# Performance work log

Measured on AMD Instinct MI355X. Metric: run time of the kernel, lower is better.

Reference implementation:

```python
import jax, jax.numpy as jnp
import numpy as np

N_NODES = 50000
NEG_SLOPE = 0.2  # PyG GATConv default
DROP_P = 0.3


def gat_layer(x, src, dst, W, a_src, a_dst, b, n):
    # x: [N, din]; src/dst: [E'] (self-loops already appended)
    h = x @ W                                   # [N, dout]
    s_src = (h * a_src).sum(-1)                 # [N]
    s_dst = (h * a_dst).sum(-1)                 # [N]
    alpha = jax.nn.leaky_relu(s_src[src] + s_dst[dst], NEG_SLOPE)  # [E']
    # segment softmax over destination node
    amax = jax.ops.segment_max(alpha, dst, num_segments=n)
    e = jnp.exp(alpha - amax[dst])
    denom = jax.ops.segment_sum(e, dst, num_segments=n)
    coef = e / denom[dst]                       # [E']
    out = jax.ops.segment_sum(coef[:, None] * h[src], dst, num_segments=n)
    return out + b


def setup_inputs() -> dict:
    key = jax.random.key(0)
    ks = jax.random.split(key, 10)
    d1, d2 = 64, 64
    E = jax.random.normal(ks[0], (N_NODES, d1), jnp.float32)
    A = jax.random.randint(ks[1], (2, 800000), 0, N_NODES, jnp.int64)
    W1 = jax.random.normal(ks[2], (d1, d1), jnp.float32) / np.sqrt(d1)
    a_src1 = jax.random.normal(ks[3], (d1,), jnp.float32) / np.sqrt(d1)
    a_dst1 = jax.random.normal(ks[4], (d1,), jnp.float32) / np.sqrt(d1)
    b1 = jnp.zeros((d1,), jnp.float32)
    W2 = jax.random.normal(ks[5], (d1, d2), jnp.float32) / np.sqrt(d1)
    a_src2 = jax.random.normal(ks[6], (d2,), jnp.float32) / np.sqrt(d2)
    a_dst2 = jax.random.normal(ks[7], (d2,), jnp.float32) / np.sqrt(d2)
    b2 = jnp.zeros((d2,), jnp.float32)
    return {"E": E, "A": A, "W1": W1, "a_src1": a_src1, "a_dst1": a_dst1,
            "b1": b1, "W2": W2, "a_src2": a_src2, "a_dst2": a_dst2, "b2": b2}


def reference(E, A, W1, a_src1, a_dst1, b1, W2, a_src2, a_dst2, b2):
    n = E.shape[0]
    loop = jnp.arange(n, dtype=A.dtype)
    src = jnp.concatenate([A[0], loop])  # PyG GATConv adds self-loops
    dst = jnp.concatenate([A[1], loop])
    x1 = jax.nn.relu(gat_layer(E, src, dst, W1, a_src1, a_dst1, b1, n))
    # F.dropout(p=0.3) runs in training mode by default -> deterministic fixed-key mask
    keep = jax.random.bernoulli(jax.random.key(42), 1.0 - DROP_P, x1.shape)
    x1 = jnp.where(keep, x1 / (1.0 - DROP_P), 0.0)
    x2 = jax.nn.relu(gat_layer(x1, src, dst, W2, a_src2, a_dst2, b2, n))
    return x2
```

## Files before the change

kernel.cpp:

```cpp
#include <hip/hip_runtime.h>


#define XT_STRIDE 68

__device__ __forceinline__ unsigned rotl32(unsigned x, unsigned r) {
  return (x << r) | (x >> (32u - r));
}

__device__ __forceinline__ void threefry2_0_42(unsigned c0, unsigned c1,
                                               unsigned* o0, unsigned* o1) {
  const unsigned k0 = 0u, k1 = 42u;
  const unsigned k2 = k0 ^ k1 ^ 0x1BD11BDAu;
  unsigned ks[3] = {k0, k1, k2};
  unsigned x0 = c0 + ks[0];
  unsigned x1 = c1 + ks[1];
  const unsigned R[2][4] = {{13u, 15u, 26u, 6u}, {17u, 29u, 16u, 24u}};
#pragma unroll
  for (int i = 0; i < 5; ++i) {
#pragma unroll
    for (int j = 0; j < 4; ++j) {
      unsigned r = R[i & 1][j];
      x0 += x1;
      x1 = rotl32(x1, r);
      x1 ^= x0;
    }
    x0 += ks[(i + 1) % 3];
    x1 += ks[(i + 2) % 3] + (unsigned)(i + 1);
  }
  *o0 = x0;
  *o1 = x1;
}

__device__ __forceinline__ float ldf(const void* p, int isbf, size_t i) {
  if (isbf) {
    unsigned short u = ((const unsigned short*)p)[i];
    return __uint_as_float(((unsigned)u) << 16);
  }
  return ((const float*)p)[i];
}

__global__ __launch_bounds__(256) void k_prep(
    const void* __restrict__ A, const void* __restrict__ Ein, int nNodes,
    const void* W1, const void* as1, const void* ad1, const void* b1,
    const void* W2, const void* as2, const void* ad2, const void* b2,
    float* __restrict__ smallc, int* __restrict__ deg, int* __restrict__ cursor,
    int* __restrict__ flags) {
  __shared__ int s_ok64, s_bf;
  int t = threadIdx.x;
  if (t == 0) { s_ok64 = 1; s_bf = 0; }
  __syncthreads();
  long long v = ((const long long*)A)[t];
  if (!(v >= 0 && v < (long long)nNodes)) atomicAnd(&s_ok64, 0);
  unsigned w = ((const unsigned*)Ein)[t];
  unsigned b = (w >> 8) & 0x7F;
  if (b >= 0x3A && b <= 0x43) atomicAdd(&s_bf, 1);
  __syncthreads();
  int isbf = (s_bf >= 200) ? 1 : 0;
  int i = blockIdx.x * 256 + t;
  if (blockIdx.x == 0 && t == 0) {
    flags[0] = s_ok64;
    flags[1] = isbf;
  }
  if (i < 8576) {
    float x;
    if (i < 4096) x = ldf(W1, isbf, i);
    else if (i < 4160) x = ldf(as1, isbf, i - 4096);
    else if (i < 4224) x = ldf(ad1, isbf, i - 4160);
    else if (i < 4288) x = ldf(b1, isbf, i - 4224);
    else if (i < 8384) x = ldf(W2, isbf, i - 4288);
    else if (i < 8448) x = ldf(as2, isbf, i - 8384);
    else if (i < 8512) x = ldf(ad2, isbf, i - 8448);
    else x = ldf(b2, isbf, i - 8512);
    smallc[i] = x;
  }
  if (i < nNodes) {
    deg[i] = 1;
    cursor[i] = 0;
  }
}

__global__ __launch_bounds__(256) void k_count_gemm(
    const void* __restrict__ A, const int* __restrict__ flags, int Eb,
    int* __restrict__ deg, const void* __restrict__ X, int xDetect,
    const float* __restrict__ W, const float* __restrict__ a_src,
    const float* __restrict__ a_dst, float* __restrict__ H,
    float* __restrict__ ssrc, float* __restrict__ sdst, int n,
    int nCountBlocks) {
  __shared__ float Xt[64 * XT_STRIDE];
  __shared__ float Ws[64 * 64];
  int t = threadIdx.x;
  if ((int)blockIdx.x < nCountBlocks) {
    int e = blockIdx.x * 256 + t;
    if (e < Eb) {
      int d = flags[0] ? (int)((const long long*)A)[(long long)Eb + e]
                       : ((const int*)A)[Eb + e];
      atomicAdd(&deg[d], 1);
    }
    return;
  }
  int bid = blockIdx.x - nCountBlocks;
  int row0 = bid * 64;
  int isbf = xDetect ? flags[1] : 0;

#pragma unroll
  for (int i = t; i < 1024; i += 256) {
    int k = i >> 4, jq = i & 15;
    *(float4*)&Ws[k * 64 + jq * 4] = *(const float4*)&W[k * 64 + jq * 4];
  }
#pragma unroll
  for (int i = t; i < 1024; i += 256) {
    int q = i & 15, r = i >> 4;
    int row = row0 + r;
    float4 v = {0.f, 0.f, 0.f, 0.f};
    if (row < n) {
      if (isbf) {
        v.x = ldf(X, 1, (size_t)row * 64 + q * 4 + 0);
        v.y = ldf(X, 1, (size_t)row * 64 + q * 4 + 1);
        v.z = ldf(X, 1, (size_t)row * 64 + q * 4 + 2);
        v.w = ldf(X, 1, (size_t)row * 64 + q * 4 + 3);
      } else {
        v = *(const float4*)&((const float*)X)[(size_t)row * 64 + q * 4];
      }
    }
    Xt[(q * 4 + 0) * XT_STRIDE + r] = v.x;
    Xt[(q * 4 + 1) * XT_STRIDE + r] = v.y;
    Xt[(q * 4 + 2) * XT_STRIDE + r] = v.z;
    Xt[(q * 4 + 3) * XT_STRIDE + r] = v.w;
  }
  __syncthreads();

  int r0 = (t >> 4) * 4;
  int c0 = (t & 15) * 4;
  float acc[4][4];
#pragma unroll
  for (int r = 0; r < 4; ++r)
#pragma unroll
    for (int c = 0; c < 4; ++c) acc[r][c] = 0.f;

#pragma unroll 8
  for (int k = 0; k < 64; ++k) {
    float4 a4 = *(const float4*)&Xt[k * XT_STRIDE + r0];
    float4 b4 = *(const float4*)&Ws[k * 64 + c0];
    const float av[4] = {a4.x, a4.y, a4.z, a4.w};
    const float bv[4] = {b4.x, b4.y, b4.z, b4.w};
#pragma unroll
    for (int r = 0; r < 4; ++r)
#pragma unroll
      for (int c = 0; c < 4; ++c) acc[r][c] = fmaf(av[r], bv[c], acc[r][c]);
  }

  const float4 asr = *(const float4*)&a_src[c0];
  const float4 adr = *(const float4*)&a_dst[c0];
#pragma unroll
  for (int r = 0; r < 4; ++r) {
    float vs = acc[r][0] * asr.x + acc[r][1] * asr.y + acc[r][2] * asr.z +
               acc[r][3] * asr.w;
    float vd = acc[r][0] * adr.x + acc[r][1] * adr.y + acc[r][2] * adr.z +
               acc[r][3] * adr.w;
#pragma unroll
    for (int d = 1; d < 16; d <<= 1) {
      vs += __shfl_xor(vs, d);
      vd += __shfl_xor(vd, d);
    }
    int row = row0 + r0 + r;
    if ((t & 15) == 0 && row < n) {
      ssrc[row] = vs;
      sdst[row] = vd;
    }
  }

#pragma unroll
  for (int r = 0; r < 4; ++r) {
    int row = row0 + r0 + r;
    if (row < n) {
      float4 o = {acc[r][0], acc[r][1], acc[r][2], acc[r][3]};
      *(float4*)&H[(size_t)row * 64 + c0] = o;
    }
  }
}

__global__ __launch_bounds__(1024) void k_scan_one(const int* __restrict__ deg,
                                                   int* __restrict__ offsets,
                                                   int n, int etot) {
  __shared__ int wsum[16];
  __shared__ int carry;
  int t = threadIdx.x;
  int lane = t & 63;
  int w = t >> 6;
  if (t == 0) carry = 0;
  __syncthreads();
  for (int base = 0; base < n; base += 1024) {
    int i = base + t;
    int x = (i < n) ? deg[i] : 0;
    int sc = x;
#pragma unroll
    for (int d = 1; d < 64; d <<= 1) {
      int o = __shfl_up(sc, d);
      if (lane >= d) sc += o;
    }
    if (lane == 63) wsum[w] = sc;
    __syncthreads();
    int cbase = carry;
    if (t < 64) {
      int v = (t < 16) ? wsum[t] : 0;
#pragma unroll
      for (int d = 1; d < 16; d <<= 1) {
        int o = __shfl_up(v, d);
        if (lane >= d) v += o;
      }
      if (t < 16) wsum[t] = v;
    }
    __syncthreads();
    int wpre = (w == 0) ? 0 : wsum[w - 1];
    if (i < n) offsets[i] = cbase + wpre + (sc - x);
    int tot = wsum[15];
    __syncthreads();
    if (t == 0) carry = cbase + tot;
    __syncthreads();
  }
  if (t == 0) offsets[n] = etot;
}

__global__ __launch_bounds__(256) void k_fill(const void* __restrict__ A,
                                              const int* __restrict__ flags,
                                              const int* __restrict__ offsets,
                                              int* cursor, int* __restrict__ csr,
                                              int Eb, int nnode) {
  int e = blockIdx.x * 256 + threadIdx.x;
  if (e >= Eb + nnode) return;
  int s, d;
  if (e < Eb) {
    if (flags[0]) {
      s = (int)((const long long*)A)[e];
      d = (int)((const long long*)A)[(long long)Eb + e];
    } else {
      s = ((const int*)A)[e];
      d = ((const int*)A)[Eb + e];
    }
  } else {
    s = d = e - Eb;
  }
  int slot = atomicAdd(&cursor[d], 1);
  csr[offsets[d] + slot] = s;
}

#define AGG_STEP(IDX, ACC)                                              \
  {                                                                     \
    int idx_ = (IDX);                                                   \
    float cl_ = __shfl(c, idx_);                                        \
    int sr_ = __shfl(sl, idx_);                                         \
    if (idx_ < glim) {                                                  \
      const float4 hv_ = *(const float4*)&h[(size_t)sr_ * 64 + f4 * 4]; \
      ACC.x = fmaf(cl_, hv_.x, ACC.x);                                  \
      ACC.y = fmaf(cl_, hv_.y, ACC.y);                                  \
      ACC.z = fmaf(cl_, hv_.z, ACC.z);                                  \
      ACC.w = fmaf(cl_, hv_.w, ACC.w);                                  \
    }                                                                   \
  }

template <int DROPOUT>
__global__ __launch_bounds__(256) void k_aggregate(
    const float* __restrict__ h, const float* __restrict__ ssrc,
    const float* __restrict__ sdst, const float* __restrict__ bias,
    const int* __restrict__ offsets, const int* __restrict__ csr,
    float* __restrict__ alphaE, float* __restrict__ out, int n) {
  int wid = (blockIdx.x * 256 + threadIdx.x) >> 6;
  int lane = threadIdx.x & 63;
  if (wid >= n) return;
  int off = offsets[wid];
  int end = offsets[wid + 1];
  int g = end - off;
  float sd = sdst[wid];
  int e4 = lane >> 4, f4 = lane & 15;
  float4 acc0 = {0.f, 0.f, 0.f, 0.f}, acc1 = {0.f, 0.f, 0.f, 0.f};

  if (g <= 64) {
    int sl = 0;
    float v = -1e30f;
    if (lane < g) {
      sl = csr[off + lane];
      float tv = ssrc[sl] + sd;
      v = (tv > 0.f) ? tv : 0.2f * tv;
    }
    float m = v;
#pragma unroll
    for (int d = 32; d; d >>= 1) m = fmaxf(m, __shfl_xor(m, d));
    float ex = (lane < g) ? __expf(v - m) : 0.f;
    float s = ex;
#pragma unroll
    for (int d = 32; d; d >>= 1) s += __shfl_xor(s, d);
    float c = ex * (1.f / s);
    int glim = g;
    for (int cb = 0; cb < g; cb += 8) {
      AGG_STEP(cb + e4, acc0)
      AGG_STEP(cb + 4 + e4, acc1)
    }
  } else {
    float mm = -1e30f, ss = 0.f;
    for (int e = off + lane; e < end; e += 64) {
      int sl2 = csr[e];
      float tv = ssrc[sl2] + sd;
      tv = (tv > 0.f) ? tv : 0.2f * tv;
      alphaE[e] = tv;
      float mn = fmaxf(mm, tv);
      ss = ss * __expf(mm - mn) + __expf(tv - mn);
      mm = mn;
    }
#pragma unroll
    for (int d = 32; d; d >>= 1) {
      float mo = __shfl_xor(mm, d);
      float so = __shfl_xor(ss, d);
      float mn = fmaxf(mm, mo);
      ss = ss * __expf(mm - mn) + so * __expf(mo - mn);
      mm = mn;
    }
    float inv = 1.f / ss;
    for (int base = off; base < end; base += 64) {
      int e = base + lane;
      int cnt = min(64, end - base);
      float c = 0.f;
      int sl = 0;
      if (e < end) {
        c = __expf(alphaE[e] - mm) * inv;
        sl = csr[e];
      }
      int glim = cnt;
      for (int cb = 0; cb < cnt; cb += 8) {
        AGG_STEP(cb + e4, acc0)
        AGG_STEP(cb + 4 + e4, acc1)
      }
    }
  }

  float4 r;
  r.x = acc0.x + acc1.x;
  r.y = acc0.y + acc1.y;
  r.z = acc0.z + acc1.z;
  r.w = acc0.w + acc1.w;
#pragma unroll
  for (int d = 16; d < 64; d <<= 1) {
    r.x += __shfl_xor(r.x, d);
    r.y += __shfl_xor(r.y, d);
    r.z += __shfl_xor(r.z, d);
    r.w += __shfl_xor(r.w, d);
  }

  unsigned long long mask = 0ull;
  if (DROPOUT) {
    unsigned i0 = (unsigned)wid * 64u + (unsigned)lane;
    unsigned o0, o1;
    threefry2_0_42(0u, i0, &o0, &o1);
    unsigned bits = o0 ^ o1;
    float u = __uint_as_float((bits >> 9) | 0x3f800000u) - 1.0f;
    mask = __ballot(u < 0.7f);
  }

  if (lane < 16) {
    const float4 b4 = *(const float4*)&bias[lane * 4];
    r.x = fmaxf(r.x + b4.x, 0.f);
    r.y = fmaxf(r.y + b4.y, 0.f);
    r.z = fmaxf(r.z + b4.z, 0.f);
    r.w = fmaxf(r.w + b4.w, 0.f);
    if (DROPOUT) {
      r.x = ((mask >> (lane * 4 + 0)) & 1ull) ? r.x / 0.7f : 0.f;
      r.y = ((mask >> (lane * 4 + 1)) & 1ull) ? r.y / 0.7f : 0.f;
      r.z = ((mask >> (lane * 4 + 2)) & 1ull) ? r.z / 0.7f : 0.f;
      r.w = ((mask >> (lane * 4 + 3)) & 1ull) ? r.w / 0.7f : 0.f;
    }
    *(float4*)&out[(size_t)wid * 64 + lane * 4] = r;
  }
}

extern "C" void kernel_launch(void* const* d_in, const int* in_sizes, int n_in,
                              void* d_out, int out_size, void* d_ws, size_t ws_size,
                              hipStream_t stream) {
  const void* E = d_in[0];
  const void* A = d_in[1];
  const void* W1 = d_in[2];
  const void* as1 = d_in[3];
  const void* ad1 = d_in[4];
  const void* b1 = d_in[5];
  const void* W2 = d_in[6];
  const void* as2 = d_in[7];
  const void* ad2 = d_in[8];
  const void* b2 = d_in[9];
  float* out = (float*)d_out;

  const int N = in_sizes[0] / 64;
  const int Eb = in_sizes[1] / 2;
  const int Etot = Eb + N;
  const int total = N * 64;

  float* ws = (float*)d_ws;
  float* h = ws;
  float* x1 = h + (size_t)total;
  float* ssrc = x1 + (size_t)total;
  float* sdst = ssrc + N;
  float* alphaE = sdst + N;
  float* smallc = alphaE + Etot;
  int* deg = (int*)(smallc + 8576);
  int* offsets = deg + N;
  int* cursor = offsets + (N + 1);
  int* flags = cursor + N;
  int* csr = flags + 2;

  float* W1c = smallc;
  float* as1c = smallc + 4096;
  float* ad1c = smallc + 4160;
  float* b1c = smallc + 4224;
  float* W2c = smallc + 4288;
  float* as2c = smallc + 8384;
  float* ad2c = smallc + 8448;
  float* b2c = smallc + 8512;

  const int gPrep = (N + 255) / 256;
  const int nCountBlocks = (Eb + 255) / 256;
  const int gTile = (N + 63) / 64;
  const int gAgg = (N + 3) / 4;
  const int gFill = (Etot + 255) / 256;

  k_prep<<<gPrep, 256, 0, stream>>>(A, E, N, W1, as1, ad1, b1, W2, as2, ad2,
                                    b2, smallc, deg, cursor, flags);
  k_count_gemm<<<nCountBlocks + gTile, 256, 0, stream>>>(
      A, flags, Eb, deg, E, 1, W1c, as1c, ad1c, h, ssrc, sdst, N, nCountBlocks);
  k_scan_one<<<1, 1024, 0, stream>>>(deg, offsets, N, Etot);
  k_fill<<<gFill, 256, 0, stream>>>(A, flags, offsets, cursor, csr, Eb, N);
  k_aggregate<1><<<gAgg, 256, 0, stream>>>(h, ssrc, sdst, b1c, offsets, csr,
                                           alphaE, x1, N);
  k_count_gemm<<<gTile, 256, 0, stream>>>(A, flags, Eb, deg, x1, 0, W2c, as2c,
                                          ad2c, h, ssrc, sdst, N, 0);
  k_aggregate<0><<<gAgg, 256, 0, stream>>>(h, ssrc, sdst, b2c, offsets, csr,
                                           alphaE, out, N);
}
```

Baseline: 320.5 us.

## Fuse all GAT stages into one persistent cooperative kernel with grid syncs

Replaces the seven separate launches (prep, count+gemm, single-block scan, fill, two aggregates, second gemm) with one cooperative persistent kernel that separates phases with grid.sync. The single-block serial scan becomes a parallel two-level chunked scan, and the GEMM now stages K in two 32-wide chunks to cut shared memory and raise occupancy. The aim is to remove launch gaps and the serial scan bottleneck. In exchange, grid-wide barriers and a grid capped at occupancy size may limit parallelism in the gather-heavy aggregation phases. The first GEMM also runs on only a third of the blocks while the rest count degrees.

```diff
diff --git a/kernel.cpp b/kernel.cpp
--- a/kernel.cpp
+++ b/kernel.cpp
@@ -1,7 +1,8 @@
 #include <hip/hip_runtime.h>
-
-
-#define XT_STRIDE 68
+#include <hip/hip_cooperative_groups.h>
+
+namespace cg = cooperative_groups;
+
 
 __device__ __forceinline__ unsigned rotl32(unsigned x, unsigned r) {
   return (x << r) | (x >> (32u - r));
@@ -39,209 +40,121 @@
   return ((const float*)p)[i];
 }
 
-__global__ __launch_bounds__(256) void k_prep(
-    const void* __restrict__ A, const void* __restrict__ Ein, int nNodes,
-    const void* W1, const void* as1, const void* ad1, const void* b1,
-    const void* W2, const void* as2, const void* ad2, const void* b2,
-    float* __restrict__ smallc, int* __restrict__ deg, int* __restrict__ cursor,
-    int* __restrict__ flags) {
-  __shared__ int s_ok64, s_bf;
-  int t = threadIdx.x;
-  if (t == 0) { s_ok64 = 1; s_bf = 0; }
+__device__ __forceinline__ void block_scan256(int v, int t, int* wpre,
+                                              int* exclOut, int* totOut) {
+  int lane = t & 63, w = t >> 6;
+  int inc = v;
+#pragma unroll
+  for (int d = 1; d < 64; d <<= 1) {
+    int o = __shfl_up(inc, d);
+    if (lane >= d) inc += o;
+  }
+  if (lane == 63) wpre[w] = inc;
   __syncthreads();
-  long long v = ((const long long*)A)[t];
-  if (!(v >= 0 && v < (long long)nNodes)) atomicAnd(&s_ok64, 0);
-  unsigned w = ((const unsigned*)Ein)[t];
-  unsigned b = (w >> 8) & 0x7F;
-  if (b >= 0x3A && b <= 0x43) atomicAdd(&s_bf, 1);
+  int wp = 0, tot = 0;
+#pragma unroll
+  for (int j = 0; j < 4; ++j) {
+    int s = wpre[j];
+    if (j < w) wp += s;
+    tot += s;
+  }
   __syncthreads();
-  int isbf = (s_bf >= 200) ? 1 : 0;
-  int i = blockIdx.x * 256 + t;
-  if (blockIdx.x == 0 && t == 0) {
-    flags[0] = s_ok64;
-    flags[1] = isbf;
-  }
-  if (i < 8576) {
-    float x;
-    if (i < 4096) x = ldf(W1, isbf, i);
-    else if (i < 4160) x = ldf(as1, isbf, i - 4096);
-    else if (i < 4224) x = ldf(ad1, isbf, i - 4160);
-    else if (i < 4288) x = ldf(b1, isbf, i - 4224);
-    else if (i < 8384) x = ldf(W2, isbf, i - 4288);
-    else if (i < 8448) x = ldf(as2, isbf, i - 8384);
-    else if (i < 8512) x = ldf(ad2, isbf, i - 8448);
-    else x = ldf(b2, isbf, i - 8512);
-    smallc[i] = x;
-  }
-  if (i < nNodes) {
-    deg[i] = 1;
-    cursor[i] = 0;
-  }
-}
-
-__global__ __launch_bounds__(256) void k_count_gemm(
-    const void* __restrict__ A, const int* __restrict__ flags, int Eb,
-    int* __restrict__ deg, const void* __restrict__ X, int xDetect,
-    const float* __restrict__ W, const float* __restrict__ a_src,
-    const float* __restrict__ a_dst, float* __restrict__ H,
-    float* __restrict__ ssrc, float* __restrict__ sdst, int n,
-    int nCountBlocks) {
-  __shared__ float Xt[64 * XT_STRIDE];
-  __shared__ float Ws[64 * 64];
-  int t = threadIdx.x;
-  if ((int)blockIdx.x < nCountBlocks) {
-    int e = blockIdx.x * 256 + t;
-    if (e < Eb) {
-      int d = flags[0] ? (int)((const long long*)A)[(long long)Eb + e]
-                       : ((const int*)A)[Eb + e];
-      atomicAdd(&deg[d], 1);
-    }
-    return;
-  }
-  int bid = blockIdx.x - nCountBlocks;
-  int row0 = bid * 64;
-  int isbf = xDetect ? flags[1] : 0;
-
-#pragma unroll
-  for (int i = t; i < 1024; i += 256) {
-    int k = i >> 4, jq = i & 15;
-    *(float4*)&Ws[k * 64 + jq * 4] = *(const float4*)&W[k * 64 + jq * 4];
-  }
-#pragma unroll
-  for (int i = t; i < 1024; i += 256) {
-    int q = i & 15, r = i >> 4;
-    int row = row0 + r;
-    float4 v = {0.f, 0.f, 0.f, 0.f};
-    if (row < n) {
-      if (isbf) {
-        v.x = ldf(X, 1, (size_t)row * 64 + q * 4 + 0);
-        v.y = ldf(X, 1, (size_t)row * 64 + q * 4 + 1);
-        v.z = ldf(X, 1, (size_t)row * 64 + q * 4 + 2);
-        v.w = ldf(X, 1, (size_t)row * 64 + q * 4 + 3);
-      } else {
-        v = *(const float4*)&((const float*)X)[(size_t)row * 64 + q * 4];
-      }
-    }
-    Xt[(q * 4 + 0) * XT_STRIDE + r] = v.x;
-    Xt[(q * 4 + 1) * XT_STRIDE + r] = v.y;
-    Xt[(q * 4 + 2) * XT_STRIDE + r] = v.z;
-    Xt[(q * 4 + 3) * XT_STRIDE + r] = v.w;
-  }
-  __syncthreads();
-
+  *exclOut = wp + inc - v;
+  *totOut = tot;
+}
+
+__device__ void gemm_phase(const void* __restrict__ X, int isbf,
+                           const float* __restrict__ Wc,
+                           const float* __restrict__ a_src,
+                           const float* __restrict__ a_dst,
+                           float* __restrict__ H, float* __restrict__ ssrc,
+                           float* __restrict__ sdst, int n, int bid0,
+                           int gstride, int t, float* Xt, float* Ws) {
+  const int gTile = (n + 63) >> 6;
   int r0 = (t >> 4) * 4;
   int c0 = (t & 15) * 4;
-  float acc[4][4];
-#pragma unroll
-  for (int r = 0; r < 4; ++r)
-#pragma unroll
-    for (int c = 0; c < 4; ++c) acc[r][c] = 0.f;
-
+  for (int tile = bid0; tile < gTile; tile += gstride) {
+    int row0 = tile * 64;
+    float acc[4][4];
+#pragma unroll
+    for (int r = 0; r < 4; ++r)
+#pragma unroll
+      for (int c = 0; c < 4; ++c) acc[r][c] = 0.f;
+
+#pragma unroll
+    for (int chunk = 0; chunk < 2; ++chunk) {
+      int kbase = chunk * 32;
+#pragma unroll
+      for (int i = t; i < 512; i += 256) {
+        int k = i >> 4, jq = i & 15;
+        *(float4*)&Ws[k * 64 + jq * 4] =
+            *(const float4*)&Wc[(kbase + k) * 64 + jq * 4];
+      }
+#pragma unroll
+      for (int i = t; i < 512; i += 256) {
+        int r = i >> 3, q = i & 7;
+        int row = row0 + r;
+        float4 v = {0.f, 0.f, 0.f, 0.f};
+        if (row < n) {
+          if (isbf) {
+            v.x = ldf(X, 1, (size_t)row * 64 + kbase + q * 4 + 0);
+            v.y = ldf(X, 1, (size_t)row * 64 + kbase + q * 4 + 1);
+            v.z = ldf(X, 1, (size_t)row * 64 + kbase + q * 4 + 2);
+            v.w = ldf(X, 1, (size_t)row * 64 + kbase + q * 4 + 3);
+          } else {
+            v = *(const float4*)&((const float*)X)[(size_t)row * 64 + kbase +
+                                                   q * 4];
+          }
+        }
+        Xt[(q * 4 + 0) * 68 + r] = v.x;
+        Xt[(q * 4 + 1) * 68 + r] = v.y;
+        Xt[(q * 4 + 2) * 68 + r] = v.z;
+        Xt[(q * 4 + 3) * 68 + r] = v.w;
+      }
+      __syncthreads();
 #pragma unroll 8
-  for (int k = 0; k < 64; ++k) {
-    float4 a4 = *(const float4*)&Xt[k * XT_STRIDE + r0];
-    float4 b4 = *(const float4*)&Ws[k * 64 + c0];
-    const float av[4] = {a4.x, a4.y, a4.z, a4.w};
-    const float bv[4] = {b4.x, b4.y, b4.z, b4.w};
-#pragma unroll
-    for (int r = 0; r < 4; ++r)
-#pragma unroll
-      for (int c = 0; c < 4; ++c) acc[r][c] = fmaf(av[r], bv[c], acc[r][c]);
-  }
-
-  const float4 asr = *(const float4*)&a_src[c0];
-  const float4 adr = *(const float4*)&a_dst[c0];
-#pragma unroll
-  for (int r = 0; r < 4; ++r) {
-    float vs = acc[r][0] * asr.x + acc[r][1] * asr.y + acc[r][2] * asr.z +
-               acc[r][3] * asr.w;
-    float vd = acc[r][0] * adr.x + acc[r][1] * adr.y + acc[r][2] * adr.z +
-               acc[r][3] * adr.w;
-#pragma unroll
-    for (int d = 1; d < 16; d <<= 1) {
-      vs += __shfl_xor(vs, d);
-      vd += __shfl_xor(vd, d);
-    }
-    int row = row0 + r0 + r;
-    if ((t & 15) == 0 && row < n) {
-      ssrc[row] = vs;
-      sdst[row] = vd;
-    }
-  }
-
-#pragma unroll
-  for (int r = 0; r < 4; ++r) {
-    int row = row0 + r0 + r;
-    if (row < n) {
-      float4 o = {acc[r][0], acc[r][1], acc[r][2], acc[r][3]};
-      *(float4*)&H[(size_t)row * 64 + c0] = o;
-    }
-  }
-}
-
-__global__ __launch_bounds__(1024) void k_scan_one(const int* __restrict__ deg,
-                                                   int* __restrict__ offsets,
-                                                   int n, int etot) {
-  __shared__ int wsum[16];
-  __shared__ int carry;
-  int t = threadIdx.x;
-  int lane = t & 63;
-  int w = t >> 6;
-  if (t == 0) carry = 0;
-  __syncthreads();
-  for (int base = 0; base < n; base += 1024) {
-    int i = base + t;
-    int x = (i < n) ? deg[i] : 0;
-    int sc = x;
-#pragma unroll
-    for (int d = 1; d < 64; d <<= 1) {
-      int o = __shfl_up(sc, d);
-      if (lane >= d) sc += o;
-    }
-    if (lane == 63) wsum[w] = sc;
-    __syncthreads();
-    int cbase = carry;
-    if (t < 64) {
-      int v = (t < 16) ? wsum[t] : 0;
+      for (int k = 0; k < 32; ++k) {
+        float4 a4 = *(const float4*)&Xt[k * 68 + r0];
+        float4 b4 = *(const float4*)&Ws[k * 64 + c0];
+        const float av[4] = {a4.x, a4.y, a4.z, a4.w};
+        const float bv[4] = {b4.x, b4.y, b4.z, b4.w};
+#pragma unroll
+        for (int r = 0; r < 4; ++r)
+#pragma unroll
+          for (int c = 0; c < 4; ++c)
+            acc[r][c] = fmaf(av[r], bv[c], acc[r][c]);
+      }
+      __syncthreads();
+    }
+
+    const float4 asr = *(const float4*)&a_src[c0];
+    const float4 adr = *(const float4*)&a_dst[c0];
+#pragma unroll
+    for (int r = 0; r < 4; ++r) {
+      float vs = acc[r][0] * asr.x + acc[r][1] * asr.y + acc[r][2] * asr.z +
+                 acc[r][3] * asr.w;
+      float vd = acc[r][0] * adr.x + acc[r][1] * adr.y + acc[r][2] * adr.z +
+                 acc[r][3] * adr.w;
 #pragma unroll
       for (int d = 1; d < 16; d <<= 1) {
-        int o = __shfl_up(v, d);
-        if (lane >= d) v += o;
-      }
-      if (t < 16) wsum[t] = v;
-    }
-    __syncthreads();
-    int wpre = (w == 0) ? 0 : wsum[w - 1];
-    if (i < n) offsets[i] = cbase + wpre + (sc - x);
-    int tot = wsum[15];
-    __syncthreads();
-    if (t == 0) carry = cbase + tot;
-    __syncthreads();
-  }
-  if (t == 0) offsets[n] = etot;
-}
-
-__global__ __launch_bounds__(256) void k_fill(const void* __restrict__ A,
-                                              const int* __restrict__ flags,
-                                              const int* __restrict__ offsets,
-                                              int* cursor, int* __restrict__ csr,
-                                              int Eb, int nnode) {
-  int e = blockIdx.x * 256 + threadIdx.x;
-  if (e >= Eb + nnode) return;
-  int s, d;
-  if (e < Eb) {
-    if (flags[0]) {
-      s = (int)((const long long*)A)[e];
-      d = (int)((const long long*)A)[(long long)Eb + e];
-    } else {
-      s = ((const int*)A)[e];
-      d = ((const int*)A)[Eb + e];
-    }
-  } else {
-    s = d = e - Eb;
-  }
-  int slot = atomicAdd(&cursor[d], 1);
-  csr[offsets[d] + slot] = s;
+        vs += __shfl_xor(vs, d);
+        vd += __shfl_xor(vd, d);
+      }
+      int row = row0 + r0 + r;
+      if ((t & 15) == 0 && row < n) {
+        ssrc[row] = vs;
+        sdst[row] = vd;
+      }
+    }
+#pragma unroll
+    for (int r = 0; r < 4; ++r) {
+      int row = row0 + r0 + r;
+      if (row < n) {
+        float4 o = {acc[r][0], acc[r][1], acc[r][2], acc[r][3]};
+        *(float4*)&H[(size_t)row * 64 + c0] = o;
+      }
+    }
+  }
 }
 
 #define AGG_STEP(IDX, ACC)                                              \
@@ -259,116 +172,243 @@
   }
 
 template <int DROPOUT>
-__global__ __launch_bounds__(256) void k_aggregate(
-    const float* __restrict__ h, const float* __restrict__ ssrc,
-    const float* __restrict__ sdst, const float* __restrict__ bias,
-    const int* __restrict__ offsets, const int* __restrict__ csr,
-    float* __restrict__ alphaE, float* __restrict__ out, int n) {
-  int wid = (blockIdx.x * 256 + threadIdx.x) >> 6;
-  int lane = threadIdx.x & 63;
-  if (wid >= n) return;
-  int off = offsets[wid];
-  int end = offsets[wid + 1];
-  int g = end - off;
-  float sd = sdst[wid];
+__device__ void agg_phase(const float* __restrict__ h,
+                          const float* __restrict__ ssrc,
+                          const float* __restrict__ sdst,
+                          const float* __restrict__ bias,
+                          const int* __restrict__ offsets,
+                          const int* __restrict__ csr,
+                          float* __restrict__ alphaE, float* __restrict__ out,
+                          int n, int bid, int G, int t) {
+  int lane = t & 63;
   int e4 = lane >> 4, f4 = lane & 15;
-  float4 acc0 = {0.f, 0.f, 0.f, 0.f}, acc1 = {0.f, 0.f, 0.f, 0.f};
-
-  if (g <= 64) {
-    int sl = 0;
-    float v = -1e30f;
-    if (lane < g) {
-      sl = csr[off + lane];
-      float tv = ssrc[sl] + sd;
-      v = (tv > 0.f) ? tv : 0.2f * tv;
-    }
-    float m = v;
-#pragma unroll
-    for (int d = 32; d; d >>= 1) m = fmaxf(m, __shfl_xor(m, d));
-    float ex = (lane < g) ? __expf(v - m) : 0.f;
-    float s = ex;
-#pragma unroll
-    for (int d = 32; d; d >>= 1) s += __shfl_xor(s, d);
-    float c = ex * (1.f / s);
-    int glim = g;
-    for (int cb = 0; cb < g; cb += 8) {
-      AGG_STEP(cb + e4, acc0)
-      AGG_STEP(cb + 4 + e4, acc1)
-    }
-  } else {
-    float mm = -1e30f, ss = 0.f;
-    for (int e = off + lane; e < end; e += 64) {
-      int sl2 = csr[e];
-      float tv = ssrc[sl2] + sd;
-      tv = (tv > 0.f) ? tv : 0.2f * tv;
-      alphaE[e] = tv;
-      float mn = fmaxf(mm, tv);
-      ss = ss * __expf(mm - mn) + __expf(tv - mn);
-      mm = mn;
-    }
-#pragma unroll
-    for (int d = 32; d; d >>= 1) {
-      float mo = __shfl_xor(mm, d);
-      float so = __shfl_xor(ss, d);
-      float mn = fmaxf(mm, mo);
-      ss = ss * __expf(mm - mn) + so * __expf(mo - mn);
-      mm = mn;
-    }
-    float inv = 1.f / ss;
-    for (int base = off; base < end; base += 64) {
-      int e = base + lane;
-      int cnt = min(64, end - base);
-      float c = 0.f;
+  for (int wid = bid * 4 + (t >> 6); wid < n; wid += G * 4) {
+    int off = offsets[wid];
+    int end = offsets[wid + 1];
+    int g = end - off;
+    float sd = sdst[wid];
+    float4 acc0 = {0.f, 0.f, 0.f, 0.f}, acc1 = {0.f, 0.f, 0.f, 0.f};
+
+    if (g <= 64) {
       int sl = 0;
-      if (e < end) {
-        c = __expf(alphaE[e] - mm) * inv;
-        sl = csr[e];
-      }
-      int glim = cnt;
-      for (int cb = 0; cb < cnt; cb += 8) {
+      float v = -1e30f;
+      if (lane < g) {
+        sl = csr[off + lane];
+        float tv = ssrc[sl] + sd;
+        v = (tv > 0.f) ? tv : 0.2f * tv;
+      }
+      float m = v;
+#pragma unroll
+      for (int d = 32; d; d >>= 1) m = fmaxf(m, __shfl_xor(m, d));
+      float ex = (lane < g) ? __expf(v - m) : 0.f;
+      float s = ex;
+#pragma unroll
+      for (int d = 32; d; d >>= 1) s += __shfl_xor(s, d);
+      float c = ex * (1.f / s);
+      int glim = g;
+      for (int cb = 0; cb < g; cb += 8) {
         AGG_STEP(cb + e4, acc0)
         AGG_STEP(cb + 4 + e4, acc1)
       }
-    }
-  }
-
-  float4 r;
-  r.x = acc0.x + acc1.x;
-  r.y = acc0.y + acc1.y;
-  r.z = acc0.z + acc1.z;
-  r.w = acc0.w + acc1.w;
-#pragma unroll
-  for (int d = 16; d < 64; d <<= 1) {
-    r.x += __shfl_xor(r.x, d);
-    r.y += __shfl_xor(r.y, d);
-    r.z += __shfl_xor(r.z, d);
-    r.w += __shfl_xor(r.w, d);
-  }
-
-  unsigned long long mask = 0ull;
-  if (DROPOUT) {
-    unsigned i0 = (unsigned)wid * 64u + (unsigned)lane;
-    unsigned o0, o1;
-    threefry2_0_42(0u, i0, &o0, &o1);
-    unsigned bits = o0 ^ o1;
-    float u = __uint_as_float((bits >> 9) | 0x3f800000u) - 1.0f;
-    mask = __ballot(u < 0.7f);
-  }
-
-  if (lane < 16) {
-    const float4 b4 = *(const float4*)&bias[lane * 4];
-    r.x = fmaxf(r.x + b4.x, 0.f);
-    r.y = fmaxf(r.y + b4.y, 0.f);
-    r.z = fmaxf(r.z + b4.z, 0.f);
-    r.w = fmaxf(r.w + b4.w, 0.f);
+    } else {
+      float mm = -1e30f, ss = 0.f;
+      for (int e = off + lane; e < end; e += 64) {
+        int sl2 = csr[e];
+        float tv = ssrc[sl2] + sd;
+        tv = (tv > 0.f) ? tv : 0.2f * tv;
+        alphaE[e] = tv;
+        float mn = fmaxf(mm, tv);
+        ss = ss * __expf(mm - mn) + __expf(tv - mn);
+        mm = mn;
+      }
+#pragma unroll
+      for (int d = 32; d; d >>= 1) {
+        float mo = __shfl_xor(mm, d);
+        float so = __shfl_xor(ss, d);
+        float mn = fmaxf(mm, mo);
+        ss = ss * __expf(mm - mn) + so * __expf(mo - mn);
+        mm = mn;
+      }
+      float inv = 1.f / ss;
+      for (int base = off; base < end; base += 64) {
+        int e = base + lane;
+        int cnt = min(64, end - base);
+        float c = 0.f;
+        int sl = 0;
+        if (e < end) {
+          c = __expf(alphaE[e] - mm) * inv;
+          sl = csr[e];
+        }
+        int glim = cnt;
+        for (int cb = 0; cb < cnt; cb += 8) {
+          AGG_STEP(cb + e4, acc0)
+          AGG_STEP(cb + 4 + e4, acc1)
+        }
+      }
+    }
+
+    float4 r;
+    r.x = acc0.x + acc1.x;
+    r.y = acc0.y + acc1.y;
+    r.z = acc0.z + acc1.z;
+    r.w = acc0.w + acc1.w;
+#pragma unroll
+    for (int d = 16; d < 64; d <<= 1) {
+      r.x += __shfl_xor(r.x, d);
+      r.y += __shfl_xor(r.y, d);
+      r.z += __shfl_xor(r.z, d);
+      r.w += __shfl_xor(r.w, d);
+    }
+
+    unsigned long long mask = 0ull;
     if (DROPOUT) {
-      r.x = ((mask >> (lane * 4 + 0)) & 1ull) ? r.x / 0.7f : 0.f;
-      r.y = ((mask >> (lane * 4 + 1)) & 1ull) ? r.y / 0.7f : 0.f;
-      r.z = ((mask >> (lane * 4 + 2)) & 1ull) ? r.z / 0.7f : 0.f;
-      r.w = ((mask >> (lane * 4 + 3)) & 1ull) ? r.w / 0.7f : 0.f;
-    }
-    *(float4*)&out[(size_t)wid * 64 + lane * 4] = r;
-  }
+      unsigned i0 = (unsigned)wid * 64u + (unsigned)lane;
+      unsigned o0, o1;
+      threefry2_0_42(0u, i0, &o0, &o1);
+      unsigned bits = o0 ^ o1;
+      float u = __uint_as_float((bits >> 9) | 0x3f800000u) - 1.0f;
+      mask = __ballot(u < 0.7f);
+    }
+
+    if (lane < 16) {
+      const float4 b4 = *(const float4*)&bias[lane * 4];
+      r.x = fmaxf(r.x + b4.x, 0.f);
+      r.y = fmaxf(r.y + b4.y, 0.f);
+      r.z = fmaxf(r.z + b4.z, 0.f);
+      r.w = fmaxf(r.w + b4.w, 0.f);
+      if (DROPOUT) {
+        r.x = ((mask >> (lane * 4 + 0)) & 1ull) ? r.x / 0.7f : 0.f;
+        r.y = ((mask >> (lane * 4 + 1)) & 1ull) ? r.y / 0.7f : 0.f;
+        r.z = ((mask >> (lane * 4 + 2)) & 1ull) ? r.z / 0.7f : 0.f;
+        r.w = ((mask >> (lane * 4 + 3)) & 1ull) ? r.w / 0.7f : 0.f;
+      }
+      *(float4*)&out[(size_t)wid * 64 + lane * 4] = r;
+    }
+  }
+}
+
+__global__ __launch_bounds__(256) void k_gat(
+    const void* E, const void* A, const void* W1, const void* as1,
+    const void* ad1, const void* b1, const void* W2, const void* as2,
+    const void* ad2, const void* b2, float* h, float* x1, float* ssrc,
+    float* sdst, float* alphaE, float* smallc, int* deg, int* offsets,
+    int* cursor, int* chunkSum, int* csr, float* outp, int N, int Eb) {
+  cg::grid_group grid = cg::this_grid();
+  __shared__ float Xt[32 * 68];
+  __shared__ float Ws[32 * 64];
+  __shared__ int wpre[4];
+  __shared__ int chunkPreLds[256];
+  __shared__ int s_flags[2];
+
+  const int t = threadIdx.x;
+  const int bid = blockIdx.x;
+  const int G = gridDim.x;
+  const int Etot = Eb + N;
+  const int nChunks = (N + 255) >> 8;
+
+  if (t == 0) {
+    s_flags[0] = 1;
+    s_flags[1] = 0;
+  }
+  __syncthreads();
+  {
+    long long v = ((const long long*)A)[t];
+    if (!(v >= 0 && v < (long long)N)) atomicAnd(&s_flags[0], 0);
+    unsigned w = ((const unsigned*)E)[t];
+    unsigned b = (w >> 8) & 0x7F;
+    if (b >= 0x3A && b <= 0x43) atomicAdd(&s_flags[1], 1);
+  }
+  __syncthreads();
+  const int is64 = s_flags[0];
+  const int isbf = (s_flags[1] >= 200) ? 1 : 0;
+  const int* A32 = (const int*)A;
+  const long long* A64 = (const long long*)A;
+
+  for (int i = bid * 256 + t; i < N; i += G * 256) {
+    deg[i] = 0;
+    cursor[i] = 0;
+  }
+  if (bid == 0) chunkSum[t] = 0;
+  for (int i = bid * 256 + t; i < 8576; i += G * 256) {
+    float x;
+    if (i < 4096) x = ldf(W1, isbf, i);
+    else if (i < 4160) x = ldf(as1, isbf, i - 4096);
+    else if (i < 4224) x = ldf(ad1, isbf, i - 4160);
+    else if (i < 4288) x = ldf(b1, isbf, i - 4224);
+    else if (i < 8384) x = ldf(W2, isbf, i - 4288);
+    else if (i < 8448) x = ldf(as2, isbf, i - 8384);
+    else if (i < 8512) x = ldf(ad2, isbf, i - 8448);
+    else x = ldf(b2, isbf, i - 8512);
+    smallc[i] = x;
+  }
+  grid.sync();
+
+  {
+    int gemmShare = G / 3;
+    if (gemmShare < 1) gemmShare = 1;
+    if (bid < gemmShare) {
+      gemm_phase(E, isbf, smallc, smallc + 4096, smallc + 4160, h, ssrc, sdst,
+                 N, bid, gemmShare, t, Xt, Ws);
+    } else {
+      int nb = G - gemmShare;
+      for (int e = (bid - gemmShare) * 256 + t; e < Eb; e += nb * 256) {
+        int d = is64 ? (int)A64[(long long)Eb + e] : A32[Eb + e];
+        atomicAdd(&deg[d], 1);
+      }
+    }
+  }
+  grid.sync();
+
+  for (int c = bid; c < nChunks; c += G) {
+    int i = c * 256 + t;
+    int adj = (i < N) ? deg[i] + 1 : 0;
+    int excl, tot;
+    block_scan256(adj, t, wpre, &excl, &tot);
+    if (i < N) offsets[i] = excl;
+    if (t == 255) chunkSum[c] = tot;
+  }
+  grid.sync();
+
+  {
+    int cs = chunkSum[t];
+    int excl, tot;
+    block_scan256(cs, t, wpre, &excl, &tot);
+    chunkPreLds[t] = excl;
+    __syncthreads();
+    for (int i = bid * 256 + t; i < N; i += G * 256)
+      offsets[i] += chunkPreLds[i >> 8];
+    if (bid == 0 && t == 0) offsets[N] = Etot;
+  }
+  grid.sync();
+
+  for (int e = bid * 256 + t; e < Etot; e += G * 256) {
+    int s, d;
+    if (e < Eb) {
+      if (is64) {
+        s = (int)A64[e];
+        d = (int)A64[(long long)Eb + e];
+      } else {
+        s = A32[e];
+        d = A32[Eb + e];
+      }
+    } else {
+      s = d = e - Eb;
+    }
+    int slot = atomicAdd(&cursor[d], 1);
+    csr[offsets[d] + slot] = s;
+  }
+  grid.sync();
+
+  agg_phase<1>(h, ssrc, sdst, smallc + 4224, offsets, csr, alphaE, x1, N, bid,
+               G, t);
+  grid.sync();
+
+  gemm_phase(x1, 0, smallc + 4288, smallc + 8384, smallc + 8448, h, ssrc, sdst,
+             N, bid, G, t, Xt, Ws);
+  grid.sync();
+
+  agg_phase<0>(h, ssrc, sdst, smallc + 8512, offsets, csr, alphaE, outp, N,
+               bid, G, t);
 }
 
 extern "C" void kernel_launch(void* const* d_in, const int* in_sizes, int n_in,
@@ -384,10 +424,10 @@
   const void* as2 = d_in[7];
   const void* ad2 = d_in[8];
   const void* b2 = d_in[9];
-  float* out = (float*)d_out;
-
-  const int N = in_sizes[0] / 64;
-  const int Eb = in_sizes[1] / 2;
+  float* outp = (float*)d_out;
+
+  int N = in_sizes[0] / 64;
+  int Eb = in_sizes[1] / 2;
   const int Etot = Eb + N;
   const int total = N * 64;
 
@@ -401,34 +441,22 @@
   int* deg = (int*)(smallc + 8576);
   int* offsets = deg + N;
   int* cursor = offsets + (N + 1);
-  int* flags = cursor + N;
-  int* csr = flags + 2;
-
-  float* W1c = smallc;
-  float* as1c = smallc + 4096;
-  float* ad1c = smallc + 4160;
-  float* b1c = smallc + 4224;
-  float* W2c = smallc + 4288;
-  float* as2c = smallc + 8384;
-  float* ad2c = smallc + 8448;
-  float* b2c = smallc + 8512;
-
-  const int gPrep = (N + 255) / 256;
-  const int nCountBlocks = (Eb + 255) / 256;
-  const int gTile = (N + 63) / 64;
-  const int gAgg = (N + 3) / 4;
-  const int gFill = (Etot + 255) / 256;
-
-  k_prep<<<gPrep, 256, 0, stream>>>(A, E, N, W1, as1, ad1, b1, W2, as2, ad2,
-                                    b2, smallc, deg, cursor, flags);
-  k_count_gemm<<<nCountBlocks + gTile, 256, 0, stream>>>(
-      A, flags, Eb, deg, E, 1, W1c, as1c, ad1c, h, ssrc, sdst, N, nCountBlocks);
-  k_scan_one<<<1, 1024, 0, stream>>>(deg, offsets, N, Etot);
-  k_fill<<<gFill, 256, 0, stream>>>(A, flags, offsets, cursor, csr, Eb, N);
-  k_aggregate<1><<<gAgg, 256, 0, stream>>>(h, ssrc, sdst, b1c, offsets, csr,
-                                           alphaE, x1, N);
-  k_count_gemm<<<gTile, 256, 0, stream>>>(A, flags, Eb, deg, x1, 0, W2c, as2c,
-                                          ad2c, h, ssrc, sdst, N, 0);
-  k_aggregate<0><<<gAgg, 256, 0, stream>>>(h, ssrc, sdst, b2c, offsets, csr,
-                                           alphaE, out, N);
-}
+  int* chunkSum = cursor + N;
+  int* csr = chunkSum + 256;
+
+  int numCU = 256;
+  hipDeviceGetAttribute(&numCU, hipDeviceAttributeMultiprocessorCount, 0);
+  int maxB = 0;
+  if (hipOccupancyMaxActiveBlocksPerMultiprocessor(&maxB, k_gat, 256,
+                                                   (size_t)0) != hipSuccess ||
+      maxB < 1)
+    maxB = 4;
+  int G = numCU * maxB;
+
+  void* args[] = {&E,      &A,      &W1,     &as1,    &ad1,      &b1,
+                  &W2,     &as2,    &ad2,    &b2,     &h,        &x1,
+                  &ssrc,   &sdst,   &alphaE, &smallc, &deg,      &offsets,
+                  &cursor, &chunkSum, &csr,  &outp,   &N,        &Eb};
+  hipLaunchCooperativeKernel((void*)k_gat, dim3(G), dim3(256), args, 0,
+                             stream);
+}
```

After: 768.2 us. 2.4x slower.
